# Kernel optimization log

Measured on AMD Instinct MI355X. Metric: run time of the kernel, lower is better.

Reference implementation:

```python
import jax, jax.numpy as jnp
import numpy as np

N_NODES = 50000
N_EDGES = 800000
IN_C, HID_C, OUT_C = 128, 64, 40


def setup_inputs() -> dict:
    key = jax.random.key(0)
    ks = jax.random.split(key, 8)
    x = jax.random.normal(ks[0], (N_NODES, IN_C), dtype=jnp.float32)
    edge_index = jax.random.randint(ks[1], (2, N_EDGES), 0, N_NODES, dtype=jnp.int32)
    # Glorot-style init for the three GCNConv linear layers (bias zero as in PyG default reset)
    def glorot(k, fan_in, fan_out):
        lim = jnp.sqrt(6.0 / (fan_in + fan_out)).astype(jnp.float32)
        return jax.random.uniform(k, (fan_in, fan_out), dtype=jnp.float32, minval=-lim, maxval=lim)
    return {
        "x": x,
        "edge_index": edge_index,
        "W1": glorot(ks[2], IN_C, HID_C), "b1": jnp.zeros((HID_C,), jnp.float32),
        "W2": glorot(ks[3], HID_C, HID_C), "b2": jnp.zeros((HID_C,), jnp.float32),
        "W3": glorot(ks[4], HID_C, OUT_C), "b3": jnp.zeros((OUT_C,), jnp.float32),
    }


def _gcn_norm(edge_index, num_nodes):
    # PyG gcn_norm: add self-loops (weight 1), symmetric D^-1/2 (A+I) D^-1/2.
    loop = jnp.arange(num_nodes, dtype=edge_index.dtype)
    row = jnp.concatenate([edge_index[0], loop])  # source
    col = jnp.concatenate([edge_index[1], loop])  # target
    w = jnp.ones(row.shape[0], dtype=jnp.float32)
    deg = jax.ops.segment_sum(w, col, num_segments=num_nodes)
    dinv = jnp.where(deg > 0, jax.lax.rsqrt(deg), 0.0)
    norm = dinv[row] * w * dinv[col]  # [E+N]
    return row, col, norm


def _gcn_conv(x, row, col, norm, W, b):
    h = x @ W                         # linear first, as in PyG GCNConv
    msg = h[row] * norm[:, None]      # gather + scale  [E+N, F]
    agg = jax.ops.segment_sum(msg, col, num_segments=x.shape[0])
    return agg + b


def reference(x, edge_index, W1, b1, W2, b2, W3, b3):
    row, col, norm = _gcn_norm(edge_index, x.shape[0])
    h = jax.nn.relu(_gcn_conv(x, row, col, norm, W1, b1))   # dropout: eval-mode identity
    h = jax.nn.relu(_gcn_conv(h, row, col, norm, W2, b2))
    h = _gcn_conv(h, row, col, norm, W3, b3)
    return jax.nn.log_softmax(h, axis=-1)
```

## Files before the change

kernel.cpp:

```cpp
#include <hip/hip_runtime.h>
#include <hip/hip_bf16.h>
#include <math.h>


#define BSHIFT 10
#define CHUNK 2048
#define CAP 24576

__global__ __launch_bounds__(64) void tinyzero_kernel(int* __restrict__ p) {
  p[threadIdx.x] = 0;
}


__global__ __launch_bounds__(256) void bucketA_kernel(const int* __restrict__ row,
                                                      const int* __restrict__ col,
                                                      int* __restrict__ bcursor,
                                                      unsigned int* __restrict__ tmp,
                                                      int e) {
  __shared__ int bcnt[64], bstart[64], bbase[64];
  __shared__ unsigned int stage[CHUNK];
  int tid = threadIdx.x;
  int base = blockIdx.x * CHUNK;
  int cnt = e - base;
  if (cnt > CHUNK) cnt = CHUNK;
  if (tid < 64) bcnt[tid] = 0;
  __syncthreads();

  unsigned int ed[CHUNK / 256];
  int rk[CHUNK / 256];
#pragma unroll
  for (int k = 0; k < CHUNK / 256; ++k) {
    int j = tid + k * 256;
    if (j < cnt) {
      int c = col[base + j], r = row[base + j];
      ed[k] = ((unsigned int)c << 16) | (unsigned int)r;
      rk[k] = atomicAdd(&bcnt[c >> BSHIFT], 1);
    }
  }
  __syncthreads();
  if (tid < 64) {
    int v = bcnt[tid];
    int run = v;
#pragma unroll
    for (int off = 1; off < 64; off <<= 1) {
      int t = __shfl_up(run, off);
      if (tid >= off) run += t;
    }
    bstart[tid] = run - v;
    if (v > 0) bbase[tid] = atomicAdd(&bcursor[tid], v);
  }
  __syncthreads();
#pragma unroll
  for (int k = 0; k < CHUNK / 256; ++k) {
    int j = tid + k * 256;
    if (j < cnt) stage[bstart[ed[k] >> (16 + BSHIFT)] + rk[k]] = ed[k];
  }
  __syncthreads();
  for (int s = tid; s < cnt; s += 256) {
    unsigned int ev = stage[s];
    int b = ev >> (16 + BSHIFT);
    tmp[(size_t)b * CAP + bbase[b] + (s - bstart[b])] = ev;
  }
}


__global__ __launch_bounds__(256) void scatterB_kernel(const unsigned int* __restrict__ tmp,
                                                       const int* __restrict__ bcursor,
                                                       int4* __restrict__ meta,
                                                       float* __restrict__ dinv,
                                                       int* __restrict__ csr, int n) {
  __shared__ int cnt[1 << BSHIFT];
  __shared__ int part[256];
  int tid = threadIdx.x;
  int b = blockIdx.x;
  int node0 = b << BSHIFT;
  int m = bcursor[b];
  const unsigned int* src = tmp + (size_t)b * CAP;

  for (int t = tid; t < (1 << BSHIFT); t += 256) cnt[t] = 0;
  __syncthreads();
  for (int i = tid; i < m; i += 256)
    atomicAdd(&cnt[(src[i] >> 16) & ((1 << BSHIFT) - 1)], 1);
  __syncthreads();

  int c0 = cnt[tid * 4 + 0], c1 = cnt[tid * 4 + 1];
  int c2 = cnt[tid * 4 + 2], c3 = cnt[tid * 4 + 3];
  int lsum = c0 + c1 + c2 + c3;
  part[tid] = lsum;
  __syncthreads();
#pragma unroll
  for (int off = 1; off < 256; off <<= 1) {
    int t = (tid >= off) ? part[tid - off] : 0;
    __syncthreads();
    part[tid] += t;
    __syncthreads();
  }
  int e0 = (tid == 0 ? 0 : part[tid - 1]);
  int e1 = e0 + c0, e2 = e1 + c1, e3 = e2 + c2;
  int base = b * CAP;

  int nd = node0 + tid * 4;
  if (nd + 0 < n) { float d = rsqrtf((float)(c0 + 1)); meta[nd + 0] = make_int4(base + e0, c0, __float_as_int(d), 0); dinv[nd + 0] = d; }
  if (nd + 1 < n) { float d = rsqrtf((float)(c1 + 1)); meta[nd + 1] = make_int4(base + e1, c1, __float_as_int(d), 0); dinv[nd + 1] = d; }
  if (nd + 2 < n) { float d = rsqrtf((float)(c2 + 1)); meta[nd + 2] = make_int4(base + e2, c2, __float_as_int(d), 0); dinv[nd + 2] = d; }
  if (nd + 3 < n) { float d = rsqrtf((float)(c3 + 1)); meta[nd + 3] = make_int4(base + e3, c3, __float_as_int(d), 0); dinv[nd + 3] = d; }
  __syncthreads();
  cnt[tid * 4 + 0] = e0; cnt[tid * 4 + 1] = e1;
  cnt[tid * 4 + 2] = e2; cnt[tid * 4 + 3] = e3;
  __syncthreads();

  for (int i = tid; i < m; i += 256) {
    unsigned int ev = src[i];
    int pos = atomicAdd(&cnt[(ev >> 16) & ((1 << BSHIFT) - 1)], 1);
    csr[base + pos] = (int)(ev & 0xFFFFu);
  }
}


__device__ __forceinline__ float bflo(unsigned int u) {
  return __uint_as_float(u << 16);
}
__device__ __forceinline__ float bfhi(unsigned int u) {
  return __uint_as_float(u & 0xffff0000u);
}
__device__ __forceinline__ unsigned int pack2bf(float a, float b) {
  __hip_bfloat16 ha = __float2bfloat16(a), hb = __float2bfloat16(b);
  unsigned short ua = *(unsigned short*)&ha, ub = *(unsigned short*)&hb;
  return (unsigned int)ua | ((unsigned int)ub << 16);
}


template <int K, int F, bool BF16IN>
__global__ __launch_bounds__(256) void gemm_kernel(const void* __restrict__ Xv,
                                                   const float* __restrict__ W,
                                                   const float* __restrict__ dinv,
                                                   __hip_bfloat16* __restrict__ Y, int n) {
  __shared__ float xs[16][K];
  int tid = threadIdx.x;
  int node0 = blockIdx.x * 16;
  if (BF16IN) {
    constexpr int KV = K / 8;
    const uint4* X4 = (const uint4*)Xv;
    for (int i = tid; i < 16 * KV; i += 256) {
      int r = i / KV, c = i % KV;
      int nd = node0 + r;
      uint4 v = make_uint4(0u, 0u, 0u, 0u);
      if (nd < n) v = X4[(size_t)nd * KV + c];
      float4 lo = make_float4(bflo(v.x), bfhi(v.x), bflo(v.y), bfhi(v.y));
      float4 hi = make_float4(bflo(v.z), bfhi(v.z), bflo(v.w), bfhi(v.w));
      ((float4*)&xs[r][0])[c * 2] = lo;
      ((float4*)&xs[r][0])[c * 2 + 1] = hi;
    }
  } else {
    constexpr int KV = K / 4;
    const float4* X4 = (const float4*)Xv;
    for (int i = tid; i < 16 * KV; i += 256) {
      int r = i / KV, c = i % KV;
      int nd = node0 + r;
      float4 v = make_float4(0.f, 0.f, 0.f, 0.f);
      if (nd < n) v = X4[(size_t)nd * KV + c];
      ((float4*)&xs[r][0])[c] = v;
    }
  }
  __syncthreads();
  int g = tid >> 6, lane = tid & 63;
  if (lane < F) {
    float acc0 = 0.f, acc1 = 0.f, acc2 = 0.f, acc3 = 0.f;
#pragma unroll 8
    for (int k = 0; k < K; ++k) {
      float w = W[k * F + lane];
      acc0 += xs[g * 4 + 0][k] * w;
      acc1 += xs[g * 4 + 1][k] * w;
      acc2 += xs[g * 4 + 2][k] * w;
      acc3 += xs[g * 4 + 3][k] * w;
    }
    float accs[4] = {acc0, acc1, acc2, acc3};
#pragma unroll
    for (int j = 0; j < 4; ++j) {
      int nd = node0 + g * 4 + j;
      if (nd < n) Y[(size_t)nd * F + lane] = __float2bfloat16(accs[j] * dinv[nd]);
    }
  }
}


template <int F, int MODE>
__global__ __launch_bounds__(256) void agg_kernel(const unsigned short* __restrict__ Hs,
                                                  const int* __restrict__ csr,
                                                  const int4* __restrict__ meta,
                                                  const float* __restrict__ bias,
                                                  void* __restrict__ Yout, int n) {
  constexpr int FO = F / 8;
  int wv = (blockIdx.x * 256 + threadIdx.x) >> 6;
  int lane = threadIdx.x & 63;
  int q = lane >> 4;
  int l16 = lane & 15;
  int sub = l16 >> 3;
  int fid = lane & 7;
  int node = wv * 4 + q;
  if (node >= n) return;
  bool activeF = (FO == 8) || (fid < FO);
  int qbase = q * 16;

  int4 mt = meta[node];
  int s = mt.x, e = mt.x + mt.y;
  float di = __int_as_float(mt.z);

  float a0 = 0.f, a1 = 0.f, a2 = 0.f, a3 = 0.f;
  float a4 = 0.f, a5 = 0.f, a6 = 0.f, a7 = 0.f;
  if (sub == 0 && activeF) {
    uint4 u = *(const uint4*)(Hs + (size_t)node * F + 8 * fid);
    a0 = bflo(u.x); a1 = bfhi(u.x); a2 = bflo(u.y); a3 = bfhi(u.y);
    a4 = bflo(u.z); a5 = bfhi(u.z); a6 = bflo(u.w); a7 = bfhi(u.w);
  }

  for (int base = s; base < e; base += 16) {
    int rem = e - base;
    int cnt = rem < 16 ? rem : 16;
    int p = csr[base + (l16 < cnt ? l16 : 0)];
    int j = 0;
    for (; j + 8 <= cnt; j += 8) {
      int r0 = __shfl(p, qbase + j + 0 + sub);
      int r1 = __shfl(p, qbase + j + 2 + sub);
      int r2 = __shfl(p, qbase + j + 4 + sub);
      int r3 = __shfl(p, qbase + j + 6 + sub);
      if (activeF) {
        uint4 u0 = *(const uint4*)(Hs + (size_t)r0 * F + 8 * fid);
        uint4 u1 = *(const uint4*)(Hs + (size_t)r1 * F + 8 * fid);
        uint4 u2 = *(const uint4*)(Hs + (size_t)r2 * F + 8 * fid);
        uint4 u3 = *(const uint4*)(Hs + (size_t)r3 * F + 8 * fid);
        a0 += bflo(u0.x); a1 += bfhi(u0.x); a2 += bflo(u0.y); a3 += bfhi(u0.y);
        a4 += bflo(u0.z); a5 += bfhi(u0.z); a6 += bflo(u0.w); a7 += bfhi(u0.w);
        a0 += bflo(u1.x); a1 += bfhi(u1.x); a2 += bflo(u1.y); a3 += bfhi(u1.y);
        a4 += bflo(u1.z); a5 += bfhi(u1.z); a6 += bflo(u1.w); a7 += bfhi(u1.w);
        a0 += bflo(u2.x); a1 += bfhi(u2.x); a2 += bflo(u2.y); a3 += bfhi(u2.y);
        a4 += bflo(u2.z); a5 += bfhi(u2.z); a6 += bflo(u2.w); a7 += bfhi(u2.w);
        a0 += bflo(u3.x); a1 += bfhi(u3.x); a2 += bflo(u3.y); a3 += bfhi(u3.y);
        a4 += bflo(u3.z); a5 += bfhi(u3.z); a6 += bflo(u3.w); a7 += bfhi(u3.w);
      }
    }
    for (; j < cnt; j += 2) {
      int idx = j + sub;
      int r = __shfl(p, qbase + (idx < cnt ? idx : j));
      if (activeF && idx < cnt) {
        uint4 u = *(const uint4*)(Hs + (size_t)r * F + 8 * fid);
        a0 += bflo(u.x); a1 += bfhi(u.x); a2 += bflo(u.y); a3 += bfhi(u.y);
        a4 += bflo(u.z); a5 += bfhi(u.z); a6 += bflo(u.w); a7 += bfhi(u.w);
      }
    }
  }

  a0 += __shfl_xor(a0, 8);
  a1 += __shfl_xor(a1, 8);
  a2 += __shfl_xor(a2, 8);
  a3 += __shfl_xor(a3, 8);
  a4 += __shfl_xor(a4, 8);
  a5 += __shfl_xor(a5, 8);
  a6 += __shfl_xor(a6, 8);
  a7 += __shfl_xor(a7, 8);

  if (MODE == 0) {
    if (sub == 0 && activeF) {
      float4 b0 = *(const float4*)(bias + 8 * fid);
      float4 b1 = *(const float4*)(bias + 8 * fid + 4);
      float v0 = a0 * di + b0.x, v1 = a1 * di + b0.y;
      float v2 = a2 * di + b0.z, v3 = a3 * di + b0.w;
      float v4 = a4 * di + b1.x, v5 = a5 * di + b1.y;
      float v6 = a6 * di + b1.z, v7 = a7 * di + b1.w;
      v0 = v0 > 0.f ? v0 : 0.f; v1 = v1 > 0.f ? v1 : 0.f;
      v2 = v2 > 0.f ? v2 : 0.f; v3 = v3 > 0.f ? v3 : 0.f;
      v4 = v4 > 0.f ? v4 : 0.f; v5 = v5 > 0.f ? v5 : 0.f;
      v6 = v6 > 0.f ? v6 : 0.f; v7 = v7 > 0.f ? v7 : 0.f;
      uint4 o;
      o.x = pack2bf(v0, v1); o.y = pack2bf(v2, v3);
      o.z = pack2bf(v4, v5); o.w = pack2bf(v6, v7);
      *(uint4*)((unsigned short*)Yout + (size_t)node * F + 8 * fid) = o;
    }
  } else {
    float v0 = -INFINITY, v1 = -INFINITY, v2 = -INFINITY, v3 = -INFINITY;
    float v4 = -INFINITY, v5 = -INFINITY, v6 = -INFINITY, v7 = -INFINITY;
    if (activeF) {
      float4 b0 = *(const float4*)(bias + 8 * fid);
      float4 b1 = *(const float4*)(bias + 8 * fid + 4);
      v0 = a0 * di + b0.x; v1 = a1 * di + b0.y;
      v2 = a2 * di + b0.z; v3 = a3 * di + b0.w;
      v4 = a4 * di + b1.x; v5 = a5 * di + b1.y;
      v6 = a6 * di + b1.z; v7 = a7 * di + b1.w;
    }
    float m = fmaxf(fmaxf(fmaxf(v0, v1), fmaxf(v2, v3)),
                    fmaxf(fmaxf(v4, v5), fmaxf(v6, v7)));
#pragma unroll
    for (int off = 4; off; off >>= 1) m = fmaxf(m, __shfl_xor(m, off));
    float ex = 0.f;
    if (activeF)
      ex = expf(v0 - m) + expf(v1 - m) + expf(v2 - m) + expf(v3 - m) +
           expf(v4 - m) + expf(v5 - m) + expf(v6 - m) + expf(v7 - m);
#pragma unroll
    for (int off = 4; off; off >>= 1) ex += __shfl_xor(ex, off);
    float lg = m + logf(ex);
    if (sub == 0 && activeF) {
      float* yp = (float*)Yout + (size_t)node * F + 8 * fid;
      *(float4*)yp = make_float4(v0 - lg, v1 - lg, v2 - lg, v3 - lg);
      *(float4*)(yp + 4) = make_float4(v4 - lg, v5 - lg, v6 - lg, v7 - lg);
    }
  }
}


extern "C" void kernel_launch(void* const* d_in, const int* in_sizes, int n_in,
                              void* d_out, int out_size, void* d_ws, size_t ws_size,
                              hipStream_t stream) {
  const float* x  = (const float*)d_in[0];
  const int*   ei = (const int*)d_in[1];
  const float* W1 = (const float*)d_in[2];
  const float* b1 = (const float*)d_in[3];
  const float* W2 = (const float*)d_in[4];
  const float* b2 = (const float*)d_in[5];
  const float* W3 = (const float*)d_in[6];
  const float* b3 = (const float*)d_in[7];
  float* out = (float*)d_out;

  const int N = in_sizes[0] / 128;
  const int E = in_sizes[1] / 2;
  const int* erow = ei;
  const int* ecol = ei + E;

  const int nbuckets = (N + (1 << BSHIFT) - 1) >> BSHIFT;

  auto align_up = [](size_t v) { return (v + 255) & ~(size_t)255; };
  char* ws = (char*)d_ws;
  size_t off = 0;
  int* bcursor  = (int*)(ws + off); off += align_up(64 * 4);
  int4* meta    = (int4*)(ws + off); off += align_up((size_t)N * 16);
  float* dinv   = (float*)(ws + off); off += align_up((size_t)N * 4);
  int* csr      = (int*)(ws + off); off += align_up((size_t)nbuckets * CAP * 4);
  unsigned int* tmp = (unsigned int*)(ws + off); off += align_up((size_t)nbuckets * CAP * 4);
  __hip_bfloat16* bufH = (__hip_bfloat16*)(ws + off); off += align_up((size_t)N * 64 * 2);
  __hip_bfloat16* bufA = (__hip_bfloat16*)(ws + off); off += align_up((size_t)N * 64 * 2);
  (void)ws_size;

  const int cb = (E + CHUNK - 1) / CHUNK;

  tinyzero_kernel<<<1, 64, 0, stream>>>(bcursor);
  bucketA_kernel<<<cb, 256, 0, stream>>>(erow, ecol, bcursor, tmp, E);
  scatterB_kernel<<<nbuckets, 256, 0, stream>>>(tmp, bcursor, meta, dinv, csr, N);

  const int gemm_blocks = (N + 15) / 16;
  const int agg_blocks = (N + 15) / 16;

  gemm_kernel<128, 64, false><<<gemm_blocks, 256, 0, stream>>>(x, W1, dinv, bufH, N);
  agg_kernel<64, 0><<<agg_blocks, 256, 0, stream>>>((const unsigned short*)bufH, csr, meta, b1, bufA, N);

  gemm_kernel<64, 64, true><<<gemm_blocks, 256, 0, stream>>>(bufA, W2, dinv, bufH, N);
  agg_kernel<64, 0><<<agg_blocks, 256, 0, stream>>>((const unsigned short*)bufH, csr, meta, b2, bufA, N);

  gemm_kernel<64, 40, true><<<gemm_blocks, 256, 0, stream>>>(bufA, W3, dinv, bufH, N);
  agg_kernel<40, 1><<<agg_blocks, 256, 0, stream>>>((const unsigned short*)bufH, csr, meta, b3, out, N);
}
```

Baseline: 165.6 us.

## Split 64-wide aggregation into two 32-feature-half passes over the CSR

Replaces the 64-feature aggregation kernel with a half-width kernel run twice, once per 32-feature half. Each wavefront then handles 8 nodes with 8 lanes per node instead of 4 nodes with 16 lanes. The intent is to shrink the gathered working set per pass (64 B per row) so each half fits better in cache, and to issue more independent gathers per lane. The cost is reading the CSR and meta twice, plus extra kernel launches.

```diff
diff --git a/kernel.cpp b/kernel.cpp
--- a/kernel.cpp
+++ b/kernel.cpp
@@ -184,12 +184,100 @@
 }
 
 
-template <int F, int MODE>
-__global__ __launch_bounds__(256) void agg_kernel(const unsigned short* __restrict__ Hs,
-                                                  const int* __restrict__ csr,
-                                                  const int4* __restrict__ meta,
-                                                  const float* __restrict__ bias,
-                                                  void* __restrict__ Yout, int n) {
+template <int FOFF>
+__global__ __launch_bounds__(256) void agg_half_kernel(
+    const unsigned short* __restrict__ Hs, const int* __restrict__ csr,
+    const int4* __restrict__ meta, const float* __restrict__ bias,
+    unsigned short* __restrict__ Yout, int n) {
+  int wv = (blockIdx.x * 256 + threadIdx.x) >> 6;
+  int lane = threadIdx.x & 63;
+  int q = lane >> 3;
+  int l8 = lane & 7;
+  int sub = l8 >> 2;
+  int fid = lane & 3;
+  int node = wv * 8 + q;
+  if (node >= n) return;
+  int qbase = q * 8;
+
+  int4 mt = meta[node];
+  int s = mt.x, e = mt.x + mt.y;
+  float di = __int_as_float(mt.z);
+
+  float a0 = 0.f, a1 = 0.f, a2 = 0.f, a3 = 0.f;
+  float a4 = 0.f, a5 = 0.f, a6 = 0.f, a7 = 0.f;
+  if (sub == 0) {
+    uint4 u = *(const uint4*)(Hs + (size_t)node * 64 + FOFF + 8 * fid);
+    a0 = bflo(u.x); a1 = bfhi(u.x); a2 = bflo(u.y); a3 = bfhi(u.y);
+    a4 = bflo(u.z); a5 = bfhi(u.z); a6 = bflo(u.w); a7 = bfhi(u.w);
+  }
+
+  for (int base = s; base < e; base += 8) {
+    int rem = e - base;
+    int cnt = rem < 8 ? rem : 8;
+    int p = csr[base + (l8 < cnt ? l8 : 0)];
+    int j = 0;
+    for (; j + 8 <= cnt; j += 8) {
+      int r0 = __shfl(p, qbase + j + 0 + sub);
+      int r1 = __shfl(p, qbase + j + 2 + sub);
+      int r2 = __shfl(p, qbase + j + 4 + sub);
+      int r3 = __shfl(p, qbase + j + 6 + sub);
+      uint4 u0 = *(const uint4*)(Hs + (size_t)r0 * 64 + FOFF + 8 * fid);
+      uint4 u1 = *(const uint4*)(Hs + (size_t)r1 * 64 + FOFF + 8 * fid);
+      uint4 u2 = *(const uint4*)(Hs + (size_t)r2 * 64 + FOFF + 8 * fid);
+      uint4 u3 = *(const uint4*)(Hs + (size_t)r3 * 64 + FOFF + 8 * fid);
+      a0 += bflo(u0.x); a1 += bfhi(u0.x); a2 += bflo(u0.y); a3 += bfhi(u0.y);
+      a4 += bflo(u0.z); a5 += bfhi(u0.z); a6 += bflo(u0.w); a7 += bfhi(u0.w);
+      a0 += bflo(u1.x); a1 += bfhi(u1.x); a2 += bflo(u1.y); a3 += bfhi(u1.y);
+      a4 += bflo(u1.z); a5 += bfhi(u1.z); a6 += bflo(u1.w); a7 += bfhi(u1.w);
+      a0 += bflo(u2.x); a1 += bfhi(u2.x); a2 += bflo(u2.y); a3 += bfhi(u2.y);
+      a4 += bflo(u2.z); a5 += bfhi(u2.z); a6 += bflo(u2.w); a7 += bfhi(u2.w);
+      a0 += bflo(u3.x); a1 += bfhi(u3.x); a2 += bflo(u3.y); a3 += bfhi(u3.y);
+      a4 += bflo(u3.z); a5 += bfhi(u3.z); a6 += bflo(u3.w); a7 += bfhi(u3.w);
+    }
+    for (; j < cnt; j += 2) {
+      int idx = j + sub;
+      int r = __shfl(p, qbase + (idx < cnt ? idx : j));
+      if (idx < cnt) {
+        uint4 u = *(const uint4*)(Hs + (size_t)r * 64 + FOFF + 8 * fid);
+        a0 += bflo(u.x); a1 += bfhi(u.x); a2 += bflo(u.y); a3 += bfhi(u.y);
+        a4 += bflo(u.z); a5 += bfhi(u.z); a6 += bflo(u.w); a7 += bfhi(u.w);
+      }
+    }
+  }
+
+  a0 += __shfl_xor(a0, 4);
+  a1 += __shfl_xor(a1, 4);
+  a2 += __shfl_xor(a2, 4);
+  a3 += __shfl_xor(a3, 4);
+  a4 += __shfl_xor(a4, 4);
+  a5 += __shfl_xor(a5, 4);
+  a6 += __shfl_xor(a6, 4);
+  a7 += __shfl_xor(a7, 4);
+
+  if (sub == 0) {
+    float4 b0 = *(const float4*)(bias + FOFF + 8 * fid);
+    float4 b1 = *(const float4*)(bias + FOFF + 8 * fid + 4);
+    float v0 = a0 * di + b0.x, v1 = a1 * di + b0.y;
+    float v2 = a2 * di + b0.z, v3 = a3 * di + b0.w;
+    float v4 = a4 * di + b1.x, v5 = a5 * di + b1.y;
+    float v6 = a6 * di + b1.z, v7 = a7 * di + b1.w;
+    v0 = v0 > 0.f ? v0 : 0.f; v1 = v1 > 0.f ? v1 : 0.f;
+    v2 = v2 > 0.f ? v2 : 0.f; v3 = v3 > 0.f ? v3 : 0.f;
+    v4 = v4 > 0.f ? v4 : 0.f; v5 = v5 > 0.f ? v5 : 0.f;
+    v6 = v6 > 0.f ? v6 : 0.f; v7 = v7 > 0.f ? v7 : 0.f;
+    uint4 o;
+    o.x = pack2bf(v0, v1); o.y = pack2bf(v2, v3);
+    o.z = pack2bf(v4, v5); o.w = pack2bf(v6, v7);
+    *(uint4*)(Yout + (size_t)node * 64 + FOFF + 8 * fid) = o;
+  }
+}
+
+
+template <int F>
+__global__ __launch_bounds__(256) void agg_final_kernel(
+    const unsigned short* __restrict__ Hs, const int* __restrict__ csr,
+    const int4* __restrict__ meta, const float* __restrict__ bias,
+    float* __restrict__ Y, int n) {
   constexpr int FO = F / 8;
   int wv = (blockIdx.x * 256 + threadIdx.x) >> 6;
   int lane = threadIdx.x & 63;
@@ -199,7 +287,7 @@
   int fid = lane & 7;
   int node = wv * 4 + q;
   if (node >= n) return;
-  bool activeF = (FO == 8) || (fid < FO);
+  bool activeF = fid < FO;
   int qbase = q * 16;
 
   int4 mt = meta[node];
@@ -259,50 +347,31 @@
   a6 += __shfl_xor(a6, 8);
   a7 += __shfl_xor(a7, 8);
 
-  if (MODE == 0) {
-    if (sub == 0 && activeF) {
-      float4 b0 = *(const float4*)(bias + 8 * fid);
-      float4 b1 = *(const float4*)(bias + 8 * fid + 4);
-      float v0 = a0 * di + b0.x, v1 = a1 * di + b0.y;
-      float v2 = a2 * di + b0.z, v3 = a3 * di + b0.w;
-      float v4 = a4 * di + b1.x, v5 = a5 * di + b1.y;
-      float v6 = a6 * di + b1.z, v7 = a7 * di + b1.w;
-      v0 = v0 > 0.f ? v0 : 0.f; v1 = v1 > 0.f ? v1 : 0.f;
-      v2 = v2 > 0.f ? v2 : 0.f; v3 = v3 > 0.f ? v3 : 0.f;
-      v4 = v4 > 0.f ? v4 : 0.f; v5 = v5 > 0.f ? v5 : 0.f;
-      v6 = v6 > 0.f ? v6 : 0.f; v7 = v7 > 0.f ? v7 : 0.f;
-      uint4 o;
-      o.x = pack2bf(v0, v1); o.y = pack2bf(v2, v3);
-      o.z = pack2bf(v4, v5); o.w = pack2bf(v6, v7);
-      *(uint4*)((unsigned short*)Yout + (size_t)node * F + 8 * fid) = o;
-    }
-  } else {
-    float v0 = -INFINITY, v1 = -INFINITY, v2 = -INFINITY, v3 = -INFINITY;
-    float v4 = -INFINITY, v5 = -INFINITY, v6 = -INFINITY, v7 = -INFINITY;
-    if (activeF) {
-      float4 b0 = *(const float4*)(bias + 8 * fid);
-      float4 b1 = *(const float4*)(bias + 8 * fid + 4);
-      v0 = a0 * di + b0.x; v1 = a1 * di + b0.y;
-      v2 = a2 * di + b0.z; v3 = a3 * di + b0.w;
-      v4 = a4 * di + b1.x; v5 = a5 * di + b1.y;
-      v6 = a6 * di + b1.z; v7 = a7 * di + b1.w;
-    }
-    float m = fmaxf(fmaxf(fmaxf(v0, v1), fmaxf(v2, v3)),
-                    fmaxf(fmaxf(v4, v5), fmaxf(v6, v7)));
-#pragma unroll
-    for (int off = 4; off; off >>= 1) m = fmaxf(m, __shfl_xor(m, off));
-    float ex = 0.f;
-    if (activeF)
-      ex = expf(v0 - m) + expf(v1 - m) + expf(v2 - m) + expf(v3 - m) +
-           expf(v4 - m) + expf(v5 - m) + expf(v6 - m) + expf(v7 - m);
-#pragma unroll
-    for (int off = 4; off; off >>= 1) ex += __shfl_xor(ex, off);
-    float lg = m + logf(ex);
-    if (sub == 0 && activeF) {
-      float* yp = (float*)Yout + (size_t)node * F + 8 * fid;
-      *(float4*)yp = make_float4(v0 - lg, v1 - lg, v2 - lg, v3 - lg);
-      *(float4*)(yp + 4) = make_float4(v4 - lg, v5 - lg, v6 - lg, v7 - lg);
-    }
+  float v0 = -INFINITY, v1 = -INFINITY, v2 = -INFINITY, v3 = -INFINITY;
+  float v4 = -INFINITY, v5 = -INFINITY, v6 = -INFINITY, v7 = -INFINITY;
+  if (activeF) {
+    float4 b0 = *(const float4*)(bias + 8 * fid);
+    float4 b1 = *(const float4*)(bias + 8 * fid + 4);
+    v0 = a0 * di + b0.x; v1 = a1 * di + b0.y;
+    v2 = a2 * di + b0.z; v3 = a3 * di + b0.w;
+    v4 = a4 * di + b1.x; v5 = a5 * di + b1.y;
+    v6 = a6 * di + b1.z; v7 = a7 * di + b1.w;
+  }
+  float m = fmaxf(fmaxf(fmaxf(v0, v1), fmaxf(v2, v3)),
+                  fmaxf(fmaxf(v4, v5), fmaxf(v6, v7)));
+#pragma unroll
+  for (int off = 4; off; off >>= 1) m = fmaxf(m, __shfl_xor(m, off));
+  float ex = 0.f;
+  if (activeF)
+    ex = expf(v0 - m) + expf(v1 - m) + expf(v2 - m) + expf(v3 - m) +
+         expf(v4 - m) + expf(v5 - m) + expf(v6 - m) + expf(v7 - m);
+#pragma unroll
+  for (int off = 4; off; off >>= 1) ex += __shfl_xor(ex, off);
+  float lg = m + logf(ex);
+  if (sub == 0 && activeF) {
+    float* yp = Y + (size_t)node * F + 8 * fid;
+    *(float4*)yp = make_float4(v0 - lg, v1 - lg, v2 - lg, v3 - lg);
+    *(float4*)(yp + 4) = make_float4(v4 - lg, v5 - lg, v6 - lg, v7 - lg);
   }
 }
 
@@ -346,14 +415,22 @@
   scatterB_kernel<<<nbuckets, 256, 0, stream>>>(tmp, bcursor, meta, dinv, csr, N);
 
   const int gemm_blocks = (N + 15) / 16;
-  const int agg_blocks = (N + 15) / 16;
+  const int agg8_blocks = (N + 31) / 32;
+  const int agg4_blocks = (N + 15) / 16;
 
   gemm_kernel<128, 64, false><<<gemm_blocks, 256, 0, stream>>>(x, W1, dinv, bufH, N);
-  agg_kernel<64, 0><<<agg_blocks, 256, 0, stream>>>((const unsigned short*)bufH, csr, meta, b1, bufA, N);
+  agg_half_kernel<0><<<agg8_blocks, 256, 0, stream>>>(
+      (const unsigned short*)bufH, csr, meta, b1, (unsigned short*)bufA, N);
+  agg_half_kernel<32><<<agg8_blocks, 256, 0, stream>>>(
+      (const unsigned short*)bufH, csr, meta, b1, (unsigned short*)bufA, N);
 
   gemm_kernel<64, 64, true><<<gemm_blocks, 256, 0, stream>>>(bufA, W2, dinv, bufH, N);
-  agg_kernel<64, 0><<<agg_blocks, 256, 0, stream>>>((const unsigned short*)bufH, csr, meta, b2, bufA, N);
+  agg_half_kernel<0><<<agg8_blocks, 256, 0, stream>>>(
+      (const unsigned short*)bufH, csr, meta, b2, (unsigned short*)bufA, N);
+  agg_half_kernel<32><<<agg8_blocks, 256, 0, stream>>>(
+      (const unsigned short*)bufH, csr, meta, b2, (unsigned short*)bufA, N);
 
   gemm_kernel<64, 40, true><<<gemm_blocks, 256, 0, stream>>>(bufA, W3, dinv, bufH, N);
-  agg_kernel<40, 1><<<agg_blocks, 256, 0, stream>>>((const unsigned short*)bufH, csr, meta, b3, out, N);
-}
+  agg_final_kernel<40><<<agg4_blocks, 256, 0, stream>>>(
+      (const unsigned short*)bufH, csr, meta, b3, out, N);
+}
```

Result: slower. 192.2 us (+16.1%).
